# Kernel tuning notes

Measured on AMD Instinct MI355X. Metric: run time of the kernel, lower is better.

Reference implementation:

```python
import jax, jax.numpy as jnp
import numpy as np

N, E, H, ED, TD = 10000, 320000, 128, 64, 32

def _lin(x, w, b):
    return x @ w + b

def _ln(x, g, b, eps=1e-5):
    m = jnp.mean(x, axis=-1, keepdims=True)
    v = jnp.var(x, axis=-1, keepdims=True)
    return (x - m) * jax.lax.rsqrt(v + eps) * g + b

def _mlp(x, w1, b1, g, bt, w2, b2):
    y = jax.nn.silu(_ln(_lin(x, w1, b1), g, bt))
    return _lin(y, w2, b2)

def setup_inputs() -> dict:
    key = jax.random.key(0)
    ks = jax.random.split(key, 32)
    s = 0.02
    nrm = lambda k, shp: jax.random.normal(k, shp, jnp.float32) * s
    d = {}
    d['h'] = jax.random.normal(ks[0], (N, H), jnp.float32)
    d['edge_attr'] = jax.random.normal(ks[1], (E, ED), jnp.float32)
    d['edge_time_emb'] = jax.random.normal(ks[2], (E, TD), jnp.float32)
    d['edge_index'] = jax.random.randint(ks[3], (2, E), 0, N)
    # edge_emb + edge_norm
    d['w_ee'] = nrm(ks[4], (ED + TD, ED)); d['b_ee'] = jnp.zeros((ED,), jnp.float32)
    d['g_en'] = jnp.ones((ED + TD,), jnp.float32); d['bt_en'] = jnp.zeros((ED + TD,), jnp.float32)
    # node_linear / bond_linear
    d['w_nl'] = nrm(ks[5], (H, H)); d['b_nl'] = jnp.zeros((H,), jnp.float32)
    d['w_bl'] = nrm(ks[6], (ED, H)); d['b_bl'] = jnp.zeros((H,), jnp.float32)
    # bond_linear_left/right, node_linear_left/right
    d['w_bll'] = nrm(ks[7], (ED, H)); d['b_bll'] = jnp.zeros((H,), jnp.float32)
    d['w_blr'] = nrm(ks[8], (ED, H)); d['b_blr'] = jnp.zeros((H,), jnp.float32)
    d['w_nll'] = nrm(ks[9], (H, H)); d['b_nll'] = jnp.zeros((H,), jnp.float32)
    d['w_nlr'] = nrm(ks[10], (H, H)); d['b_nlr'] = jnp.zeros((H,), jnp.float32)
    # left / right MLPs: Linear(2H,H), LayerNorm(H), SiLU, Linear(H,H)
    d['mlpl_w1'] = nrm(ks[11], (2 * H, H)); d['mlpl_b1'] = jnp.zeros((H,), jnp.float32)
    d['mlpl_g'] = jnp.ones((H,), jnp.float32); d['mlpl_bt'] = jnp.zeros((H,), jnp.float32)
    d['mlpl_w2'] = nrm(ks[12], (H, H)); d['mlpl_b2'] = jnp.zeros((H,), jnp.float32)
    d['mlpr_w1'] = nrm(ks[13], (2 * H, H)); d['mlpr_b1'] = jnp.zeros((H,), jnp.float32)
    d['mlpr_g'] = jnp.ones((H,), jnp.float32); d['mlpr_bt'] = jnp.zeros((H,), jnp.float32)
    d['mlpr_w2'] = nrm(ks[14], (H, H)); d['mlpr_b2'] = jnp.zeros((H,), jnp.float32)
    # layer_norm(3H) + bond_out: Linear(3H,H), SiLU, Linear(H,ED)
    d['g_ln'] = jnp.ones((3 * H,), jnp.float32); d['bt_ln'] = jnp.zeros((3 * H,), jnp.float32)
    d['w_o1'] = nrm(ks[15], (3 * H, H)); d['b_o1'] = jnp.zeros((H,), jnp.float32)
    d['w_o2'] = nrm(ks[16], (H, ED)); d['b_o2'] = jnp.zeros((ED,), jnp.float32)
    return d

def reference(h, edge_attr, edge_time_emb, edge_index,
              w_ee, b_ee, g_en, bt_en, w_nl, b_nl, w_bl, b_bl,
              w_bll, b_bll, w_blr, b_blr, w_nll, b_nll, w_nlr, b_nlr,
              mlpl_w1, mlpl_b1, mlpl_g, mlpl_bt, mlpl_w2, mlpl_b2,
              mlpr_w1, mlpr_b1, mlpr_g, mlpr_bt, mlpr_w2, mlpr_b2,
              g_ln, bt_ln, w_o1, b_o1, w_o2, b_o2):
    src, dst = edge_index[0], edge_index[1]
    n = h.shape[0]
    # edge_attr = edge_emb(edge_norm(cat([edge_attr, edge_time_emb])))
    ea = _lin(_ln(jnp.concatenate([edge_attr, edge_time_emb], axis=-1), g_en, bt_en), w_ee, b_ee)
    # node linears applied per-node then gathered (same math as gather-then-linear)
    x_i = _lin(h, w_nll, b_nll)[src]            # [E, H]
    x_j = _lin(h, w_nlr, b_nlr)[dst]            # [E, H]
    edge_i = _lin(ea, w_bll, b_bll)             # [E, H]
    edge_j = _lin(ea, w_blr, b_blr)             # [E, H]
    inter_i = _mlp(jnp.concatenate([edge_i, x_i], axis=-1), mlpl_w1, mlpl_b1, mlpl_g, mlpl_bt, mlpl_w2, mlpl_b2)
    inter_j = _mlp(jnp.concatenate([edge_j, x_j], axis=-1), mlpr_w1, mlpr_b1, mlpr_g, mlpr_bt, mlpr_w2, mlpr_b2)
    # scatter_sum to nodes, then regather on the same index
    inter_i = jax.ops.segment_sum(inter_i, src, num_segments=n)[src]
    inter_j = jax.ops.segment_sum(inter_j, dst, num_segments=n)[dst]
    h_node = _lin(h, w_nl, b_nl)
    h_bond = jnp.concatenate([inter_i + inter_j, h_node[src] + h_node[dst], _lin(ea, w_bl, b_bl)], axis=-1)  # [E, 3H]
    h_bond = _ln(h_bond, g_ln, bt_ln)
    out = _lin(jax.nn.silu(_lin(h_bond, w_o1, b_o1)), w_o2, b_o2)  # [E, ED]
    return out
```

## Files before the change

### kernel.cpp

```cpp
#include <hip/hip_runtime.h>
#include <math.h>


using u16 = unsigned short;
using u32 = unsigned int;
typedef __attribute__((ext_vector_type(8))) short  short8;
typedef __attribute__((ext_vector_type(4))) float  f32x4;
typedef __attribute__((ext_vector_type(4))) u32    uint4v;
typedef __attribute__((ext_vector_type(2))) u32    uint2v;

constexpr int NN = 10000;
constexpr int EE = 320000;
constexpr int MAXDEG = 96;

__device__ __forceinline__ float b2f(u16 v) {
  return __builtin_bit_cast(float, (u32)v << 16);
}
__device__ __forceinline__ float b2f_lo(u32 v) {
  return __builtin_bit_cast(float, v << 16);
}
__device__ __forceinline__ float b2f_hi(u32 v) {
  return __builtin_bit_cast(float, v & 0xffff0000u);
}
__device__ __forceinline__ u32 cvtpk(float lo, float hi) {
  u32 r;
  asm("v_cvt_pk_bf16_f32 %0, %1, %2" : "=v"(r) : "v"(lo), "v"(hi));
  return r;
}
__device__ __forceinline__ u16 f2b(float f) {
  return (u16)cvtpk(f, f);
}
__device__ __forceinline__ uint2v pack4(f32x4 v) {
  uint2v r;
  r.x = cvtpk(v[0], v[1]);
  r.y = cvtpk(v[2], v[3]);
  return r;
}
__device__ __forceinline__ u32 addpk(u32 a, u32 b) {
  return cvtpk(b2f_lo(a) + b2f_lo(b), b2f_hi(a) + b2f_hi(b));
}
__device__ __forceinline__ float silu_f(float v) {
  return v * __builtin_amdgcn_rcpf(1.f + __expf(-v));
}
template<typename T>
__device__ __forceinline__ T ntld(const T* p) { return __builtin_nontemporal_load(p); }
template<typename T>
__device__ __forceinline__ void ntst(T* p, T v) { __builtin_nontemporal_store(v, p); }

struct Params {
  const void* h; const void* edge_attr; const void* te;
  const int* eidx;
  const int* flag;
  const u16 *b_ee, *g_en, *bt_en;
  const u16 *b_nl, *b_bl, *b_bll, *b_blr, *b_nll, *b_nlr;
  const u16 *l_b1, *l_g, *l_bt, *l_b2;
  const u16 *r_b1, *r_g, *r_bt, *r_b2;
  const u16 *g_ln, *bt_ln, *b_o1, *b_o2;
  const u16 *w_eeT, *w_blT, *w_bllT, *w_blrT, *w_nlT, *w_nllT, *w_nlrT;
  const u16 *l_w1T, *l_w2T, *r_w1T, *r_w2T, *o1T, *o2T;
  u16 *a_nll, *a_nlr, *tbl_i, *ea_ws;
  u32 *cnt0, *cnt1, *elist0, *elist1;
  u16 *accb_j;
  float *accf_i, *accf_j;
  u16 *inter0, *inter1;
  int amode;
  void *out;
};

__global__ __launch_bounds__(256) void k_sniff(const u16* p, int* flag)
{
  __shared__ int c;
  if (threadIdx.x == 0) c = 0;
  __syncthreads();
  u16 v = p[threadIdx.x * 2];
  int e = (v >> 7) & 0xff;
  if (e >= 100 && e <= 140) atomicAdd(&c, 1);
  __syncthreads();
  if (threadIdx.x == 0) *flag = (c >= 200) ? 1 : 0;
}

template<int K, int CT, int RT>
__device__ __forceinline__ void wave_gemm(const u16* A, int SA,
                                          const u16* __restrict__ BT,
                                          f32x4 (&acc)[RT][CT], int n0)
{
  const int lane = threadIdx.x & 63;
  const int quad = lane >> 4, l16 = lane & 15;
  constexpr int NKT = K / 32;
  short8 b[CT], bn[CT], a[RT], an[RT];
  const int k0 = quad * 8;
#pragma unroll
  for (int c = 0; c < CT; ++c)
    b[c] = *(const short8*)(BT + (size_t)(n0 + c * 16 + l16) * K + k0);
#pragma unroll
  for (int rt = 0; rt < RT; ++rt)
    a[rt] = *(const short8*)(A + (rt * 16 + l16) * SA + k0);
#pragma unroll
  for (int kt = 0; kt < NKT; ++kt) {
    if (kt + 1 < NKT) {
      const int k1 = (kt + 1) * 32 + quad * 8;
#pragma unroll
      for (int c = 0; c < CT; ++c)
        bn[c] = *(const short8*)(BT + (size_t)(n0 + c * 16 + l16) * K + k1);
#pragma unroll
      for (int rt = 0; rt < RT; ++rt)
        an[rt] = *(const short8*)(A + (rt * 16 + l16) * SA + k1);
    }
#pragma unroll
    for (int rt = 0; rt < RT; ++rt)
#pragma unroll
      for (int c = 0; c < CT; ++c)
        acc[rt][c] = __builtin_amdgcn_mfma_f32_16x16x32_bf16(a[rt], b[c], acc[rt][c], 0, 0, 0);
    if (kt + 1 < NKT) {
#pragma unroll
      for (int c = 0; c < CT; ++c) b[c] = bn[c];
#pragma unroll
      for (int rt = 0; rt < RT; ++rt) a[rt] = an[rt];
    }
  }
}

template<int CT, int RT, bool SILU>
__device__ __forceinline__ void epi_lds(f32x4 (&acc)[RT][CT], u16* O, int SO,
                                        int outc0, const u16* __restrict__ bias,
                                        int biasc0)
{
  const int lane = threadIdx.x & 63;
  const int quad = lane >> 4, l16 = lane & 15;
#pragma unroll
  for (int c = 0; c < CT; ++c) {
    float bv = b2f(bias[biasc0 + c * 16 + l16]);
#pragma unroll
    for (int rt = 0; rt < RT; ++rt) {
#pragma unroll
      for (int r = 0; r < 4; ++r) {
        float v = acc[rt][c][r] + bv;
        if (SILU) v = silu_f(v);
        O[(rt * 16 + quad * 4 + r) * SO + outc0 + c * 16 + l16] = f2b(v);
      }
    }
  }
}

template<int D, int ROWS, bool SILU>
__device__ __forceinline__ void ln_rows(u16* buf, int S,
                                        const u16* __restrict__ g,
                                        const u16* __restrict__ bt, float* red)
{
  constexpr int P = 256 / ROWS;
  constexpr int C = D / P;
  constexpr int NV = C / 8;
  const int t = threadIdx.x;
  const int row = t / P, p = t % P;
  u16* r = buf + row * S + p * C;
  uint4v vv[NV];
  float s = 0.f, ss = 0.f;
#pragma unroll
  for (int n = 0; n < NV; ++n) {
    vv[n] = *(const uint4v*)(r + n * 8);
#pragma unroll
    for (int q = 0; q < 4; ++q) {
      float lo = b2f_lo(vv[n][q]), hi = b2f_hi(vv[n][q]);
      s += lo + hi;
      ss += lo * lo + hi * hi;
    }
  }
  red[row * 2 * P + p] = s;
  red[row * 2 * P + P + p] = ss;
  __syncthreads();
  float S1 = 0.f, S2 = 0.f;
#pragma unroll
  for (int q = 0; q < P / 4; ++q) {
    f32x4 x = *(const f32x4*)&red[row * 2 * P + q * 4];
    f32x4 y = *(const f32x4*)&red[row * 2 * P + P + q * 4];
    S1 += x[0] + x[1] + x[2] + x[3];
    S2 += y[0] + y[1] + y[2] + y[3];
  }
  const float mean = S1 / (float)D;
  const float var  = S2 / (float)D - mean * mean;
  const float rstd = rsqrtf(var + 1e-5f);
#pragma unroll
  for (int n = 0; n < NV; ++n) {
    uint4v gv = *(const uint4v*)(g + p * C + n * 8);
    uint4v bv = *(const uint4v*)(bt + p * C + n * 8);
    uint4v ov;
#pragma unroll
    for (int q = 0; q < 4; ++q) {
      float lo = (b2f_lo(vv[n][q]) - mean) * rstd * b2f_lo(gv[q]) + b2f_lo(bv[q]);
      float hi = (b2f_hi(vv[n][q]) - mean) * rstd * b2f_hi(gv[q]) + b2f_hi(bv[q]);
      if (SILU) { lo = silu_f(lo); hi = silu_f(hi); }
      ov[q] = cvtpk(lo, hi);
    }
    *(uint4v*)(r + n * 8) = ov;
  }
  __syncthreads();
}

struct TDesc { const void* s; u16* d; int K; int N; };
struct TArgs { TDesc t[34]; const int* flag; };

__global__ __launch_bounds__(256) void k_transpose(TArgs a)
{
  const int flag = *a.flag;
  TDesc dsc = a.t[blockIdx.y];
  const int total = dsc.K * dsc.N;
  for (int i = blockIdx.x * 256 + threadIdx.x; i < total; i += gridDim.x * 256) {
    int n = i / dsc.K;
    int k = i - n * dsc.K;
    size_t si = (size_t)k * dsc.N + n;
    dsc.d[i] = flag ? ((const u16*)dsc.s)[si] : f2b(((const float*)dsc.s)[si]);
  }
}

__global__ __launch_bounds__(256) void k_hist(const int* eidx, u32* cnt0,
                                              u32* elist0, u32* cnt1, u32* elist1)
{
  int e = blockIdx.x * 256 + threadIdx.x;
  if (e >= EE) return;
  int n0 = eidx[e];
  u32 p0 = atomicAdd(&cnt0[n0], 1u);
  if (p0 < MAXDEG) elist0[(size_t)n0 * MAXDEG + p0] = (u32)e;
  int n1 = eidx[EE + e];
  u32 p1 = atomicAdd(&cnt1[n1], 1u);
  if (p1 < MAXDEG) elist1[(size_t)n1 * MAXDEG + p1] = (u32)e;
}

__global__ __launch_bounds__(256) void k_node(Params a)
{
  __shared__ __align__(16) u16 hs[64 * 136];
  const int tid = threadIdx.x, w = tid >> 6;
  const int n0 = blockIdx.x * 64;
  const int flag = *a.flag;
  if (flag) {
    for (int c = tid; c < 1024; c += 256) {
      int row = c >> 4, cc = c & 15;
      int node = n0 + row;
      uint4v v = {};
      if (node < NN) v = ntld((const uint4v*)((const u16*)a.h + (size_t)node * 128 + cc * 8));
      *(uint4v*)&hs[row * 136 + cc * 8] = v;
    }
  } else {
    for (int c = tid; c < 2048; c += 256) {
      int row = c >> 5, cc = c & 31;
      int node = n0 + row;
      uint2v pk = {};
      if (node < NN) {
        f32x4 fv = ntld((const f32x4*)((const float*)a.h + (size_t)node * 128 + cc * 4));
        pk = pack4(fv);
      }
      *(uint2v*)&hs[row * 136 + cc * 4] = pk;
    }
  }
  __syncthreads();
  const u16* wT[3] = { a.w_nllT, a.w_nlrT, a.w_nlT };
  const u16* bs[3] = { a.b_nll, a.b_nlr, a.b_nl };
  u16* os[3] = { a.a_nll, a.a_nlr, a.tbl_i + 128 };
  const int st[3] = { 128, 128, 256 };
  const int lane = tid & 63, quad = lane >> 4, l16 = lane & 15;
#pragma unroll 1
  for (int m = 0; m < 3; ++m) {
    f32x4 acc[4][2] = {};
    wave_gemm<128, 2, 4>(hs, 136, wT[m], acc, w * 32);
#pragma unroll
    for (int c = 0; c < 2; ++c) {
      int col = w * 32 + c * 16 + l16;
      float bv = b2f(bs[m][col]);
#pragma unroll
      for (int rt = 0; rt < 4; ++rt) {
#pragma unroll
        for (int r = 0; r < 4; ++r) {
          int node = n0 + rt * 16 + quad * 4 + r;
          if (node < NN) os[m][(size_t)node * st[m] + col] = f2b(acc[rt][c][r] + bv);
        }
      }
    }
  }
}

__global__ __launch_bounds__(256) void k_ea(Params a)
{
  __shared__ __align__(16) u16 u[64 * 104];
  __shared__ __align__(16) u16 eas[64 * 72];
  __shared__ float red[512];
  const int tid = threadIdx.x, w = tid >> 6;
  const int e0 = blockIdx.x * 64;
  const int flag = *a.flag;
  if (flag) {
    for (int c = tid; c < 512; c += 256) {
      int row = c >> 3, cc = c & 7;
      *(uint4v*)&u[row * 104 + cc * 8] =
          ntld((const uint4v*)((const u16*)a.edge_attr + (size_t)(e0 + row) * 64 + cc * 8));
    }
    {
      int row = tid >> 2, cc = tid & 3;
      *(uint4v*)&u[row * 104 + 64 + cc * 8] =
          ntld((const uint4v*)((const u16*)a.te + (size_t)(e0 + row) * 32 + cc * 8));
    }
  } else {
    for (int c = tid; c < 1024; c += 256) {
      int row = c >> 4, cc = c & 15;
      f32x4 fv = ntld((const f32x4*)((const float*)a.edge_attr + (size_t)(e0 + row) * 64 + cc * 4));
      *(uint2v*)&u[row * 104 + cc * 4] = pack4(fv);
    }
    for (int c = tid; c < 512; c += 256) {
      int row = c >> 3, cc = c & 7;
      f32x4 fv = ntld((const f32x4*)((const float*)a.te + (size_t)(e0 + row) * 32 + cc * 4));
      *(uint2v*)&u[row * 104 + 64 + cc * 4] = pack4(fv);
    }
  }
  __syncthreads();
  ln_rows<96, 64, false>(u, 104, a.g_en, a.bt_en, red);
  {
    f32x4 acc[4][1] = {};
    wave_gemm<96, 1, 4>(u, 104, a.w_eeT, acc, w * 16);
    epi_lds<1, 4, false>(acc, eas, 72, w * 16, a.b_ee, w * 16);
  }
  __syncthreads();
  for (int c = tid; c < 512; c += 256) {
    int row = c >> 3, cc = c & 7;
    *(uint4v*)(a.ea_ws + (size_t)(e0 + row) * 64 + cc * 8) =
        *(const uint4v*)&eas[row * 72 + cc * 8];
  }
}

template<bool ATOMIC>
__global__ __launch_bounds__(256, 4) void k_mlp(
    const u16* __restrict__ ea_ws, const int* __restrict__ eidx_side,
    const u16* __restrict__ an, const u16* __restrict__ wbT,
    const u16* __restrict__ bb, const u16* __restrict__ w1T,
    const u16* __restrict__ b1, const u16* __restrict__ gg,
    const u16* __restrict__ bt, const u16* __restrict__ w2T,
    const u16* __restrict__ b2, u16* __restrict__ inter,
    float* __restrict__ accf)
{
  __shared__ __align__(16) u16 u[64 * 264];
  __shared__ float red[512];
  __shared__ int sidx[64];
  const int tid = threadIdx.x, w = tid >> 6;
  const int e0 = blockIdx.x * 64;
  const int lane = tid & 63, quad = lane >> 4, l16 = lane & 15;

  if (tid < 64) sidx[tid] = eidx_side[e0 + tid];
  __syncthreads();
  for (int c = tid; c < 1024; c += 256) {
    int row = c >> 4, cc = c & 15;
    *(uint4v*)&u[row * 264 + 128 + cc * 8] =
        *(const uint4v*)(an + (size_t)sidx[row] * 128 + cc * 8);
  }
  {
    f32x4 acc[4][2] = {};
    wave_gemm<64, 2, 4>(ea_ws + (size_t)e0 * 64, 64, wbT, acc, w * 32);
    epi_lds<2, 4, false>(acc, u, 264, w * 32, bb, w * 32);
  }
  __syncthreads();
  {
    f32x4 acc[4][2] = {};
    wave_gemm<256, 2, 4>(u, 264, w1T, acc, w * 32);
    __syncthreads();
    epi_lds<2, 4, false>(acc, u, 264, w * 32, b1, w * 32);
  }
  __syncthreads();
  ln_rows<128, 64, true>(u, 264, gg, bt, red);
  {
    f32x4 acc[4][2] = {};
    wave_gemm<128, 2, 4>(u, 264, w2T, acc, w * 32);
    if (ATOMIC) {
#pragma unroll
      for (int c = 0; c < 2; ++c) {
        int col = w * 32 + c * 16 + l16;
        float bias = b2f(b2[col]);
#pragma unroll
        for (int rt = 0; rt < 4; ++rt)
#pragma unroll
          for (int r = 0; r < 4; ++r) {
            int row = rt * 16 + quad * 4 + r;
            unsafeAtomicAdd(accf + (size_t)sidx[row] * 128 + col,
                            acc[rt][c][r] + bias);
          }
      }
    } else {
      epi_lds<2, 4, false>(acc, u, 264, 128 + w * 32, b2, w * 32);
      __syncthreads();
      for (int c = tid; c < 1024; c += 256) {
        int row = c >> 4, cc = c & 15;
        ntst((uint4v*)(inter + (size_t)(e0 + row) * 128 + cc * 8),
             *(const uint4v*)&u[row * 264 + 128 + cc * 8]);
      }
    }
  }
}

__global__ __launch_bounds__(256) void k_nodesum(const u16* __restrict__ inter,
                                                 const u32* __restrict__ cnt,
                                                 const u32* __restrict__ elist,
                                                 u16* __restrict__ dst, int dstride)
{
  const int wv = (blockIdx.x * 256 + threadIdx.x) >> 6;
  const int lane = threadIdx.x & 63;
  if (wv >= NN) return;
  u32 deg = cnt[wv];
  if (deg > MAXDEG) deg = MAXDEG;
  const u32* el = elist + (size_t)wv * MAXDEG;
  float s0 = 0.f, s1 = 0.f;
  u32 d = 0;
  for (; d + 4 <= deg; d += 4) {
    uint4v ev = ntld((const uint4v*)(el + d));
    u32 v0 = ntld((const u32*)(inter + (size_t)ev[0] * 128 + lane * 2));
    u32 v1 = ntld((const u32*)(inter + (size_t)ev[1] * 128 + lane * 2));
    u32 v2 = ntld((const u32*)(inter + (size_t)ev[2] * 128 + lane * 2));
    u32 v3 = ntld((const u32*)(inter + (size_t)ev[3] * 128 + lane * 2));
    s0 += b2f_lo(v0) + b2f_lo(v1) + b2f_lo(v2) + b2f_lo(v3);
    s1 += b2f_hi(v0) + b2f_hi(v1) + b2f_hi(v2) + b2f_hi(v3);
  }
  for (; d < deg; ++d) {
    u32 e = el[d];
    u32 v = ntld((const u32*)(inter + (size_t)e * 128 + lane * 2));
    s0 += b2f_lo(v);
    s1 += b2f_hi(v);
  }
  *(u32*)(dst + (size_t)wv * dstride + lane * 2) = cvtpk(s0, s1);
}

__global__ __launch_bounds__(256, 4) void k_stage2(Params a)
{
  __shared__ __align__(16) u16 bond[32 * 392];
  __shared__ float red[512];
  __shared__ int sidx[2][32];
  const int tid = threadIdx.x, w = tid >> 6;
  const int e0 = blockIdx.x * 32;
  const int flag = *a.flag;
  const int lane = tid & 63, quad = lane >> 4, l16 = lane & 15;

  if (tid < 64) {
    int side = tid >> 5, i = tid & 31;
    sidx[side][i] = a.eidx[(size_t)side * EE + e0 + i];
  }
  __syncthreads();
  if (a.amode) {
    for (int c = tid; c < 1024; c += 256) {
      int row = c >> 5, cc = c & 31;
      const u16* ps = a.tbl_i + (size_t)sidx[0][row] * 256 + cc * 8;
      const u16* pp = (cc < 16)
          ? a.accb_j + (size_t)sidx[1][row] * 128 + cc * 8
          : a.tbl_i + (size_t)sidx[1][row] * 256 + cc * 8;
      uint4v vs = *(const uint4v*)ps;
      uint4v vp = *(const uint4v*)pp;
      uint4v ov;
#pragma unroll
      for (int q = 0; q < 4; ++q) ov[q] = addpk(vs[q], vp[q]);
      *(uint4v*)&bond[row * 392 + cc * 8] = ov;
    }
  } else {
    for (int c = tid; c < 1024; c += 256) {
      int row = c >> 5, cc = c & 31;
      f32x4 vi = *(const f32x4*)(a.accf_i + (size_t)sidx[0][row] * 128 + cc * 4);
      f32x4 vj = *(const f32x4*)(a.accf_j + (size_t)sidx[1][row] * 128 + cc * 4);
      f32x4 sm = vi + vj;
      *(uint2v*)&bond[row * 392 + cc * 4] = pack4(sm);
    }
    for (int c = tid; c < 512; c += 256) {
      int row = c >> 4, cc = c & 15;
      uint4v hs = *(const uint4v*)(a.tbl_i + (size_t)sidx[0][row] * 256 + 128 + cc * 8);
      uint4v hd = *(const uint4v*)(a.tbl_i + (size_t)sidx[1][row] * 256 + 128 + cc * 8);
      uint4v ov;
#pragma unroll
      for (int q = 0; q < 4; ++q) ov[q] = addpk(hs[q], hd[q]);
      *(uint4v*)&bond[row * 392 + 128 + cc * 8] = ov;
    }
  }
  {
    f32x4 acc[2][2] = {};
    wave_gemm<64, 2, 2>(a.ea_ws + (size_t)e0 * 64, 64, a.w_blT, acc, w * 32);
    epi_lds<2, 2, false>(acc, bond, 392, 256 + w * 32, a.b_bl, w * 32);
  }
  __syncthreads();
  ln_rows<384, 32, false>(bond, 392, a.g_ln, a.bt_ln, red);
  {
    f32x4 acc[2][2] = {};
    wave_gemm<384, 2, 2>(bond, 392, a.o1T, acc, w * 32);
    __syncthreads();
    epi_lds<2, 2, true>(acc, bond, 392, w * 32, a.b_o1, w * 32);
  }
  __syncthreads();
  {
    f32x4 acc[2][1] = {};
    wave_gemm<128, 1, 2>(bond, 392, a.o2T, acc, w * 16);
    if (flag) {
      epi_lds<1, 2, false>(acc, bond, 392, 128 + w * 16, a.b_o2, w * 16);
      __syncthreads();
      for (int c = tid; c < 256; c += 256) {
        int row = c >> 3, cc = c & 7;
        ntst((uint4v*)((u16*)a.out + (size_t)(e0 + row) * 64 + cc * 8),
             *(const uint4v*)&bond[row * 392 + 128 + cc * 8]);
      }
    } else {
      float bvv = b2f(a.b_o2[w * 16 + l16]);
#pragma unroll
      for (int rt = 0; rt < 2; ++rt)
#pragma unroll
        for (int r = 0; r < 4; ++r) {
          int row = rt * 16 + quad * 4 + r;
          ((float*)((char*)bond + (size_t)row * 784 + 272))[w * 16 + l16] =
              acc[rt][0][r] + bvv;
        }
      __syncthreads();
      for (int c = tid; c < 512; c += 256) {
        int row = c >> 4, cc = c & 15;
        f32x4 v = *(const f32x4*)((char*)bond + (size_t)row * 784 + 272 + cc * 16);
        ntst((f32x4*)((float*)a.out + (size_t)(e0 + row) * 64 + cc * 4), v);
      }
    }
  }
}

extern "C" void kernel_launch(void* const* d_in, const int* in_sizes, int n_in,
                              void* d_out, int out_size, void* d_ws, size_t ws_size,
                              hipStream_t stream)
{
  char* ws = (char*)d_ws;

  const size_t O_EET  = 0;
  const size_t O_BLT  = 12288;
  const size_t O_BLLT = O_BLT  + 16384;
  const size_t O_BLRT = O_BLLT + 16384;
  const size_t O_NLT  = O_BLRT + 16384;
  const size_t O_NLLT = O_NLT  + 32768;
  const size_t O_NLRT = O_NLLT + 32768;
  const size_t O_LW1T = O_NLRT + 32768;
  const size_t O_LW2T = O_LW1T + 65536;
  const size_t O_RW1T = O_LW2T + 32768;
  const size_t O_RW2T = O_RW1T + 65536;
  const size_t O_O1T  = O_RW2T + 32768;
  const size_t O_O2T  = O_O1T  + 98304;
  const size_t PRM    = O_O2T  + 16384;
  const size_t FLAG   = PRM + 6016;
  const size_t A_NLL  = PRM + 6144;
  const size_t A_NLR  = A_NLL + 2560000;
  const size_t TBL_I  = A_NLR + 2560000;
  const size_t EA     = TBL_I + 5120000;
  const size_t TAIL   = EA + 40960000;
  const size_t ACCF_I = TAIL;
  const size_t ACCF_J = TAIL + 5120000;
  const size_t NEED_ATOM = TAIL + 10240000;
  const size_t CNT0   = TAIL;
  const size_t CNT1   = TAIL + 40960;
  const size_t EL0    = TAIL + 81920;
  const size_t EL1    = EL0 + 3840000;
  const size_t ACCB_J = EL1 + 3840000;
  const size_t INTER0 = ACCB_J + 2560000;
  const size_t NEED_CSR = INTER0 + 81920000;
  if (ws_size < NEED_ATOM) return;
  const int amode = (ws_size >= NEED_CSR) ? 1 : 0;

  const size_t pOff[21] = { 0, 128, 320, 512, 768, 1024, 1280, 1536, 1792,
                            2048, 2304, 2560, 2816, 3072, 3328, 3584, 3840,
                            4096, 4864, 5632, 5888 };
  const int   pIdx[21] = { 5, 6, 7, 9, 11, 13, 15, 17, 19,
                           21, 22, 23, 25, 27, 28, 29, 31,
                           32, 33, 35, 37 };
  const int   pLen[21] = { 64, 96, 96, 128, 128, 128, 128, 128, 128,
                           128, 128, 128, 128, 128, 128, 128, 128,
                           384, 384, 128, 64 };
  auto P = [&](int slot) { return (const u16*)(ws + PRM + pOff[slot]); };

  Params a;
  a.h = d_in[0]; a.edge_attr = d_in[1]; a.te = d_in[2];
  a.eidx = (const int*)d_in[3];
  a.flag = (const int*)(ws + FLAG);
  a.b_ee = P(0); a.g_en = P(1); a.bt_en = P(2);
  a.b_nl = P(3); a.b_bl = P(4); a.b_bll = P(5); a.b_blr = P(6);
  a.b_nll = P(7); a.b_nlr = P(8);
  a.l_b1 = P(9); a.l_g = P(10); a.l_bt = P(11); a.l_b2 = P(12);
  a.r_b1 = P(13); a.r_g = P(14); a.r_bt = P(15); a.r_b2 = P(16);
  a.g_ln = P(17); a.bt_ln = P(18); a.b_o1 = P(19); a.b_o2 = P(20);
  a.w_eeT = (const u16*)(ws + O_EET);   a.w_blT  = (const u16*)(ws + O_BLT);
  a.w_bllT = (const u16*)(ws + O_BLLT); a.w_blrT = (const u16*)(ws + O_BLRT);
  a.w_nlT = (const u16*)(ws + O_NLT);   a.w_nllT = (const u16*)(ws + O_NLLT);
  a.w_nlrT = (const u16*)(ws + O_NLRT);
  a.l_w1T = (const u16*)(ws + O_LW1T);  a.l_w2T = (const u16*)(ws + O_LW2T);
  a.r_w1T = (const u16*)(ws + O_RW1T);  a.r_w2T = (const u16*)(ws + O_RW2T);
  a.o1T = (const u16*)(ws + O_O1T);     a.o2T = (const u16*)(ws + O_O2T);
  a.a_nll = (u16*)(ws + A_NLL); a.a_nlr = (u16*)(ws + A_NLR);
  a.tbl_i = (u16*)(ws + TBL_I); a.ea_ws = (u16*)(ws + EA);
  a.cnt0 = (u32*)(ws + CNT0); a.cnt1 = (u32*)(ws + CNT1);
  a.elist0 = (u32*)(ws + EL0); a.elist1 = (u32*)(ws + EL1);
  a.accb_j = (u16*)(ws + ACCB_J);
  a.accf_i = (float*)(ws + ACCF_I); a.accf_j = (float*)(ws + ACCF_J);
  a.inter0 = (u16*)(ws + INTER0); a.inter1 = (u16*)(ws + INTER0);
  a.amode = amode;
  a.out = d_out;

  TArgs ta;
  ta.flag = (const int*)(ws + FLAG);
  ta.t[0]  = { d_in[4],  (u16*)(ws + O_EET),  96, 64 };
  ta.t[1]  = { d_in[10], (u16*)(ws + O_BLT),  64, 128 };
  ta.t[2]  = { d_in[12], (u16*)(ws + O_BLLT), 64, 128 };
  ta.t[3]  = { d_in[14], (u16*)(ws + O_BLRT), 64, 128 };
  ta.t[4]  = { d_in[8],  (u16*)(ws + O_NLT),  128, 128 };
  ta.t[5]  = { d_in[16], (u16*)(ws + O_NLLT), 128, 128 };
  ta.t[6]  = { d_in[18], (u16*)(ws + O_NLRT), 128, 128 };
  ta.t[7]  = { d_in[20], (u16*)(ws + O_LW1T), 256, 128 };
  ta.t[8]  = { d_in[24], (u16*)(ws + O_LW2T), 128, 128 };
  ta.t[9]  = { d_in[26], (u16*)(ws + O_RW1T), 256, 128 };
  ta.t[10] = { d_in[30], (u16*)(ws + O_RW2T), 128, 128 };
  ta.t[11] = { d_in[34], (u16*)(ws + O_O1T),  384, 128 };
  ta.t[12] = { d_in[36], (u16*)(ws + O_O2T),  128, 64 };
  for (int s = 0; s < 21; ++s)
    ta.t[13 + s] = { d_in[pIdx[s]], (u16*)(ws + PRM + pOff[s]), 1, pLen[s] };

  k_sniff<<<1, 256, 0, stream>>>((const u16*)d_in[1], (int*)(ws + FLAG));
  if (amode) hipMemsetAsync(ws + CNT0, 0, 81920, stream);
  else       hipMemsetAsync(ws + ACCF_I, 0, 10240000, stream);
  k_transpose<<<dim3(16, 34), 256, 0, stream>>>(ta);
  if (amode)
    k_hist<<<(EE + 255) / 256, 256, 0, stream>>>(a.eidx, a.cnt0, a.elist0, a.cnt1, a.elist1);
  k_node<<<(NN + 63) / 64, 256, 0, stream>>>(a);
  k_ea<<<EE / 64, 256, 0, stream>>>(a);

  if (amode) {
    k_mlp<false><<<EE / 64, 256, 0, stream>>>(a.ea_ws, a.eidx, a.a_nll, a.w_bllT,
        a.b_bll, a.l_w1T, a.l_b1, a.l_g, a.l_bt, a.l_w2T, a.l_b2, a.inter0, nullptr);
    k_nodesum<<<(NN * 64 + 255) / 256, 256, 0, stream>>>(a.inter0, a.cnt0, a.elist0,
        a.tbl_i, 256);
    k_mlp<false><<<EE / 64, 256, 0, stream>>>(a.ea_ws, a.eidx + EE, a.a_nlr, a.w_blrT,
        a.b_blr, a.r_w1T, a.r_b1, a.r_g, a.r_bt, a.r_w2T, a.r_b2, a.inter1, nullptr);
    k_nodesum<<<(NN * 64 + 255) / 256, 256, 0, stream>>>(a.inter1, a.cnt1, a.elist1,
        a.accb_j, 128);
  } else {
    k_mlp<true><<<EE / 64, 256, 0, stream>>>(a.ea_ws, a.eidx, a.a_nll, a.w_bllT,
        a.b_bll, a.l_w1T, a.l_b1, a.l_g, a.l_bt, a.l_w2T, a.l_b2, nullptr, a.accf_i);
    k_mlp<true><<<EE / 64, 256, 0, stream>>>(a.ea_ws, a.eidx + EE, a.a_nlr, a.w_blrT,
        a.b_blr, a.r_w1T, a.r_b1, a.r_g, a.r_bt, a.r_w2T, a.r_b2, nullptr, a.accf_j);
  }
  k_stage2<<<EE / 32, 256, 0, stream>>>(a);
}
```

Baseline: 755.0 us.

## Fuse edge MLP with per-node CSR reduction, dropping intermediate edge buffer

```diff
diff --git a/kernel.cpp b/kernel.cpp
--- a/kernel.cpp
+++ b/kernel.cpp
@@ -62,7 +62,6 @@
   u32 *cnt0, *cnt1, *elist0, *elist1;
   u16 *accb_j;
   float *accf_i, *accf_j;
-  u16 *inter0, *inter1;
   int amode;
   void *out;
 };
@@ -323,15 +322,92 @@
   }
 }
 
-template<bool ATOMIC>
-__global__ __launch_bounds__(256, 4) void k_mlp(
+__global__ __launch_bounds__(256, 6) void k_mlp_csr(
+    const u16* __restrict__ ea_ws, const u32* __restrict__ cnt,
+    const u32* __restrict__ elist, const u16* __restrict__ an,
+    const u16* __restrict__ wbT, const u16* __restrict__ bb,
+    const u16* __restrict__ w1T, const u16* __restrict__ b1,
+    const u16* __restrict__ gg, const u16* __restrict__ bt,
+    const u16* __restrict__ w2T, const u16* __restrict__ b2,
+    u16* __restrict__ dst, int dstride)
+{
+  __shared__ __align__(16) u16 u[32 * 264];
+  __shared__ __align__(16) u16 eas[32 * 72];
+  __shared__ float red[512];
+  __shared__ u32 sel[MAXDEG];
+  const int tid = threadIdx.x, w = tid >> 6;
+  const int n = blockIdx.x;
+  const int lane = tid & 63, quad = lane >> 4, l16 = lane & 15;
+
+  u32 deg = cnt[n];
+  if (deg > MAXDEG) deg = MAXDEG;
+  if (tid < MAXDEG && (u32)tid < deg)
+    sel[tid] = ntld(elist + (size_t)n * MAXDEG + tid);
+  for (int c = tid; c < 512; c += 256) {
+    int row = c >> 4, cc = c & 15;
+    uint4v xv = *(const uint4v*)(an + (size_t)n * 128 + cc * 8);
+    *(uint4v*)&u[row * 264 + 128 + cc * 8] = xv;
+  }
+  __syncthreads();
+
+  float s[2] = { 0.f, 0.f };
+  for (u32 c0 = 0; c0 < deg; c0 += 32) {
+    int rem = (int)(deg - c0); if (rem > 32) rem = 32;
+    {
+      int row = tid >> 3, cc = tid & 7;
+      u32 e = sel[c0 + (row < rem ? row : 0)];
+      *(uint4v*)&eas[row * 72 + cc * 8] =
+          ntld((const uint4v*)(ea_ws + (size_t)e * 64 + cc * 8));
+    }
+    __syncthreads();
+    {
+      f32x4 acc[2][2] = {};
+      wave_gemm<64, 2, 2>(eas, 72, wbT, acc, w * 32);
+      epi_lds<2, 2, false>(acc, u, 264, w * 32, bb, w * 32);
+    }
+    __syncthreads();
+    {
+      f32x4 acc[2][2] = {};
+      wave_gemm<256, 2, 2>(u, 264, w1T, acc, w * 32);
+      __syncthreads();
+      epi_lds<2, 2, false>(acc, u, 264, w * 32, b1, w * 32);
+    }
+    __syncthreads();
+    ln_rows<128, 32, true>(u, 264, gg, bt, red);
+    {
+      f32x4 acc[2][2] = {};
+      wave_gemm<128, 2, 2>(u, 264, w2T, acc, w * 32);
+#pragma unroll
+      for (int c = 0; c < 2; ++c)
+#pragma unroll
+        for (int rt = 0; rt < 2; ++rt)
+#pragma unroll
+          for (int r = 0; r < 4; ++r) {
+            int row = rt * 16 + quad * 4 + r;
+            s[c] += (row < rem) ? acc[rt][c][r] : 0.f;
+          }
+    }
+    __syncthreads();
+  }
+#pragma unroll
+  for (int c = 0; c < 2; ++c) {
+    float v = s[c];
+    v += __shfl_xor(v, 16);
+    v += __shfl_xor(v, 32);
+    if (quad == 0) {
+      int col = w * 32 + c * 16 + l16;
+      dst[(size_t)n * dstride + col] = f2b(v + (float)deg * b2f(b2[col]));
+    }
+  }
+}
+
+__global__ __launch_bounds__(256, 4) void k_mlp_atomic(
     const u16* __restrict__ ea_ws, const int* __restrict__ eidx_side,
     const u16* __restrict__ an, const u16* __restrict__ wbT,
     const u16* __restrict__ bb, const u16* __restrict__ w1T,
     const u16* __restrict__ b1, const u16* __restrict__ gg,
     const u16* __restrict__ bt, const u16* __restrict__ w2T,
-    const u16* __restrict__ b2, u16* __restrict__ inter,
-    float* __restrict__ accf)
+    const u16* __restrict__ b2, float* __restrict__ accf)
 {
   __shared__ __align__(16) u16 u[64 * 264];
   __shared__ float red[512];
@@ -364,61 +440,20 @@
   {
     f32x4 acc[4][2] = {};
     wave_gemm<128, 2, 4>(u, 264, w2T, acc, w * 32);
-    if (ATOMIC) {
-#pragma unroll
-      for (int c = 0; c < 2; ++c) {
-        int col = w * 32 + c * 16 + l16;
-        float bias = b2f(b2[col]);
-#pragma unroll
-        for (int rt = 0; rt < 4; ++rt)
-#pragma unroll
-          for (int r = 0; r < 4; ++r) {
-            int row = rt * 16 + quad * 4 + r;
-            unsafeAtomicAdd(accf + (size_t)sidx[row] * 128 + col,
-                            acc[rt][c][r] + bias);
-          }
-      }
-    } else {
-      epi_lds<2, 4, false>(acc, u, 264, 128 + w * 32, b2, w * 32);
-      __syncthreads();
-      for (int c = tid; c < 1024; c += 256) {
-        int row = c >> 4, cc = c & 15;
-        ntst((uint4v*)(inter + (size_t)(e0 + row) * 128 + cc * 8),
-             *(const uint4v*)&u[row * 264 + 128 + cc * 8]);
-      }
-    }
-  }
-}
-
-__global__ __launch_bounds__(256) void k_nodesum(const u16* __restrict__ inter,
-                                                 const u32* __restrict__ cnt,
-                                                 const u32* __restrict__ elist,
-                                                 u16* __restrict__ dst, int dstride)
-{
-  const int wv = (blockIdx.x * 256 + threadIdx.x) >> 6;
-  const int lane = threadIdx.x & 63;
-  if (wv >= NN) return;
-  u32 deg = cnt[wv];
-  if (deg > MAXDEG) deg = MAXDEG;
-  const u32* el = elist + (size_t)wv * MAXDEG;
-  float s0 = 0.f, s1 = 0.f;
-  u32 d = 0;
-  for (; d + 4 <= deg; d += 4) {
-    uint4v ev = ntld((const uint4v*)(el + d));
-    u32 v0 = ntld((const u32*)(inter + (size_t)ev[0] * 128 + lane * 2));
-    u32 v1 = ntld((const u32*)(inter + (size_t)ev[1] * 128 + lane * 2));
-    u32 v2 = ntld((const u32*)(inter + (size_t)ev[2] * 128 + lane * 2));
-    u32 v3 = ntld((const u32*)(inter + (size_t)ev[3] * 128 + lane * 2));
-    s0 += b2f_lo(v0) + b2f_lo(v1) + b2f_lo(v2) + b2f_lo(v3);
-    s1 += b2f_hi(v0) + b2f_hi(v1) + b2f_hi(v2) + b2f_hi(v3);
-  }
-  for (; d < deg; ++d) {
-    u32 e = el[d];
-    u32 v = ntld((const u32*)(inter + (size_t)e * 128 + lane * 2));
-    s0 += b2f_lo(v);
-    s1 += b2f_hi(v);
-  }
-  *(u32*)(dst + (size_t)wv * dstride + lane * 2) = cvtpk(s0, s1);
+#pragma unroll
+    for (int c = 0; c < 2; ++c) {
+      int col = w * 32 + c * 16 + l16;
+      float bias = b2f(b2[col]);
+#pragma unroll
+      for (int rt = 0; rt < 4; ++rt)
+#pragma unroll
+        for (int r = 0; r < 4; ++r) {
+          int row = rt * 16 + quad * 4 + r;
+          unsafeAtomicAdd(accf + (size_t)sidx[row] * 128 + col,
+                          acc[rt][c][r] + bias);
+        }
+    }
+  }
 }
 
 __global__ __launch_bounds__(256, 4) void k_stage2(Params a)
@@ -547,8 +582,7 @@
   const size_t EL0    = TAIL + 81920;
   const size_t EL1    = EL0 + 3840000;
   const size_t ACCB_J = EL1 + 3840000;
-  const size_t INTER0 = ACCB_J + 2560000;
-  const size_t NEED_CSR = INTER0 + 81920000;
+  const size_t NEED_CSR = ACCB_J + 2560000;
   if (ws_size < NEED_ATOM) return;
   const int amode = (ws_size >= NEED_CSR) ? 1 : 0;
 
@@ -586,7 +620,6 @@
   a.elist0 = (u32*)(ws + EL0); a.elist1 = (u32*)(ws + EL1);
   a.accb_j = (u16*)(ws + ACCB_J);
   a.accf_i = (float*)(ws + ACCF_I); a.accf_j = (float*)(ws + ACCF_J);
-  a.inter0 = (u16*)(ws + INTER0); a.inter1 = (u16*)(ws + INTER0);
   a.amode = amode;
   a.out = d_out;
 
@@ -618,19 +651,17 @@
   k_ea<<<EE / 64, 256, 0, stream>>>(a);
 
   if (amode) {
-    k_mlp<false><<<EE / 64, 256, 0, stream>>>(a.ea_ws, a.eidx, a.a_nll, a.w_bllT,
-        a.b_bll, a.l_w1T, a.l_b1, a.l_g, a.l_bt, a.l_w2T, a.l_b2, a.inter0, nullptr);
-    k_nodesum<<<(NN * 64 + 255) / 256, 256, 0, stream>>>(a.inter0, a.cnt0, a.elist0,
+    k_mlp_csr<<<NN, 256, 0, stream>>>(a.ea_ws, a.cnt0, a.elist0, a.a_nll,
+        a.w_bllT, a.b_bll, a.l_w1T, a.l_b1, a.l_g, a.l_bt, a.l_w2T, a.l_b2,
         a.tbl_i, 256);
-    k_mlp<false><<<EE / 64, 256, 0, stream>>>(a.ea_ws, a.eidx + EE, a.a_nlr, a.w_blrT,
-        a.b_blr, a.r_w1T, a.r_b1, a.r_g, a.r_bt, a.r_w2T, a.r_b2, a.inter1, nullptr);
-    k_nodesum<<<(NN * 64 + 255) / 256, 256, 0, stream>>>(a.inter1, a.cnt1, a.elist1,
+    k_mlp_csr<<<NN, 256, 0, stream>>>(a.ea_ws, a.cnt1, a.elist1, a.a_nlr,
+        a.w_blrT, a.b_blr, a.r_w1T, a.r_b1, a.r_g, a.r_bt, a.r_w2T, a.r_b2,
         a.accb_j, 128);
   } else {
-    k_mlp<true><<<EE / 64, 256, 0, stream>>>(a.ea_ws, a.eidx, a.a_nll, a.w_bllT,
-        a.b_bll, a.l_w1T, a.l_b1, a.l_g, a.l_bt, a.l_w2T, a.l_b2, nullptr, a.accf_i);
-    k_mlp<true><<<EE / 64, 256, 0, stream>>>(a.ea_ws, a.eidx + EE, a.a_nlr, a.w_blrT,
-        a.b_blr, a.r_w1T, a.r_b1, a.r_g, a.r_bt, a.r_w2T, a.r_b2, nullptr, a.accf_j);
+    k_mlp_atomic<<<EE / 64, 256, 0, stream>>>(a.ea_ws, a.eidx, a.a_nll, a.w_bllT,
+        a.b_bll, a.l_w1T, a.l_b1, a.l_g, a.l_bt, a.l_w2T, a.l_b2, a.accf_i);
+    k_mlp_atomic<<<EE / 64, 256, 0, stream>>>(a.ea_ws, a.eidx + EE, a.a_nlr, a.w_blrT,
+        a.b_blr, a.r_w1T, a.r_b1, a.r_g, a.r_bt, a.r_w2T, a.r_b2, a.accf_j);
   }
   k_stage2<<<EE / 32, 256, 0, stream>>>(a);
 }
```

Result: slower. 1.030 ms (+36.4%).
